# Kernel tuning notes

Hardware: AMD Instinct MI355X
Metric: run time of the kernel (lower is better)

The kernel has to match this reference:

```python
import jax, jax.numpy as jnp
import numpy as np

B, N, DIM, H, DH = 2, 4096, 512, 8, 64  # inner_dim = H*DH = 512


def setup_inputs() -> dict:
    key = jax.random.key(0)
    ks = jax.random.split(key, 4)
    x = jax.random.normal(ks[0], (B, N, DIM), dtype=jnp.float32)
    Wq = jax.random.normal(ks[1], (DIM, H * DH), dtype=jnp.float32) * (DIM ** -0.5)
    Wkv = jax.random.normal(ks[2], (DIM, 2 * H * DH), dtype=jnp.float32) * (DIM ** -0.5)
    Wo = jax.random.normal(ks[3], (H * DH, DIM), dtype=jnp.float32) * ((H * DH) ** -0.5)
    bo = jnp.zeros((DIM,), dtype=jnp.float32)
    return {"x": x, "Wq": Wq, "Wkv": Wkv, "Wo": Wo, "bo": bo}


def reference(x, Wq, Wkv, Wo, bo):
    scale = DH ** -0.5
    # projections (context defaults to x -> self-attention)
    q = x @ Wq
    kv = x @ Wkv
    k, v = jnp.split(kv, 2, axis=-1)
    # NOTE: original code scales q by dim_head**-0.5 in forward() AND again
    # inside attention(), i.e. an effective dim_head**-1 scaling. Faithful.
    q = q * scale
    # b n (h d) -> b h n d
    split_heads = lambda t: t.reshape(B, N, H, DH).transpose(0, 2, 1, 3)
    q, k, v = map(split_heads, (q, k, v))
    q = q * scale  # second scaling inside attention()
    sim = jnp.einsum('bhid,bhjd->bhij', q, k)  # [B,H,N,N] full score matrix
    sim = sim - jax.lax.stop_gradient(jnp.max(sim, axis=-1, keepdims=True))
    mask_value = -jnp.finfo(sim.dtype).max
    causal_mask = jnp.triu(jnp.ones((N, N), dtype=bool), k=1)
    sim = jnp.where(causal_mask, mask_value, sim)
    attn = jax.nn.softmax(sim, axis=-1)
    out = jnp.einsum('bhij,bhjd->bhid', attn, v)
    out = out.transpose(0, 2, 1, 3).reshape(B, N, H * DH)  # b h n d -> b n (h d)
    return out @ Wo + bo
```

## Files before the change

### kernel.cpp

```cpp
#include <hip/hip_runtime.h>

typedef short s16x8 __attribute__((ext_vector_type(8)));
typedef float f32x4 __attribute__((ext_vector_type(4)));
typedef unsigned short u16;
typedef unsigned int u32;

#define MFMA16(a, b, c) __builtin_amdgcn_mfma_f32_16x16x32_bf16((a), (b), (c), 0, 0, 0)

__device__ __forceinline__ u16 f2bf(float f) {
  u32 u = __float_as_uint(f);
  u += 0x7fffu + ((u >> 16) & 1u);
  return (u16)(u >> 16);
}
__device__ __forceinline__ u16 f2bf_fast(float f) {
  return (u16)((__float_as_uint(f) + 0x8000u) >> 16);
}
__device__ __forceinline__ float ex2(float x) {
  float r;
  asm("v_exp_f32 %0, %1" : "=v"(r) : "v"(x));
  return r;
}
__device__ __forceinline__ void gll(const u16* g, u16* l) {
  __builtin_amdgcn_global_load_lds((const __attribute__((address_space(1))) u32*)g,
                                   (__attribute__((address_space(3))) u32*)l, 16, 0, 0);
}

__global__ __launch_bounds__(256) void k_prep(const float* __restrict__ x,
                                              const float* __restrict__ Wq,
                                              const float* __restrict__ Wkv,
                                              const float* __restrict__ Wo,
                                              u16* __restrict__ xb,
                                              u16* __restrict__ wqkvt,
                                              u16* __restrict__ wot) {
  const int bx = blockIdx.x, t = threadIdx.x;
  if (bx < 4096) {
    int i = bx * 256 + t;
    float4 v = ((const float4*)x)[i];
    ushort4 o;
    o.x = f2bf(v.x); o.y = f2bf(v.y); o.z = f2bf(v.z); o.w = f2bf(v.w);
    ((ushort4*)xb)[i] = o;
    return;
  }
  __shared__ u16 tl[64 * 66];
  const float* src; u16* dst; int N, kb, nb;
  if (bx < 4160)      { int tb = bx - 4096; src = Wq;  dst = wqkvt;          N = 512;  kb = tb >> 3; nb = tb & 7; }
  else if (bx < 4288) { int tb = bx - 4160; src = Wkv; dst = wqkvt + 262144; N = 1024; kb = tb >> 4; nb = tb & 15; }
  else                { int tb = bx - 4288; src = Wo;  dst = wot;            N = 512;  kb = tb >> 3; nb = tb & 7; }
#pragma unroll
  for (int it = 0; it < 4; ++it) {
    int idx = it * 256 + t;
    int kl = idx >> 4, nc = idx & 15;
    float4 v = *(const float4*)(src + (kb * 64 + kl) * N + nb * 64 + nc * 4);
    u16* p = &tl[kl * 66 + nc * 4];
    p[0] = f2bf(v.x); p[1] = f2bf(v.y); p[2] = f2bf(v.z); p[3] = f2bf(v.w);
  }
  __syncthreads();
#pragma unroll
  for (int it = 0; it < 2; ++it) {
    int idx = it * 256 + t;
    int nl = idx >> 3, kc = idx & 7;
    u16 tmp[8];
#pragma unroll
    for (int j = 0; j < 8; ++j) tmp[j] = tl[(kc * 8 + j) * 66 + nl];
    *(s16x8*)(dst + (nb * 64 + nl) * 512 + kb * 64 + kc * 8) = *(const s16x8*)tmp;
  }
}

__global__ __launch_bounds__(256, 2) void k_gemm_qkv(
    const u16* __restrict__ A, const u16* __restrict__ Bt,
    u16* __restrict__ Qb, u16* __restrict__ Kb, u16* __restrict__ Vt) {
  __shared__ __align__(16) u16 As[8192], Bs[8192];
  const int t = threadIdx.x, w = t >> 6, l = t & 63, quad = l >> 4, lr = l & 15;
  const int bm = blockIdx.x, bn = blockIdx.y;
  const int wm = (w >> 1) * 64, wn = (w & 1) * 64;
  const f32x4 fz = {0.f, 0.f, 0.f, 0.f};
  f32x4 acc[4][4];
#pragma unroll
  for (int i = 0; i < 4; ++i)
#pragma unroll
    for (int j = 0; j < 4; ++j) acc[i][j] = fz;
  const u16* Ag = A + bm * 128 * 512;
  const u16* Bg = Bt + bn * 128 * 512;
  for (int kk = 0; kk < 8; ++kk) {
    __syncthreads();
#pragma unroll
    for (int i = 0; i < 4; ++i) {
      int ci = w * 256 + i * 64 + l;
      int row = ci >> 3, cb = ci & 7;
      int off = row * 512 + kk * 64 + ((cb ^ (row & 7)) << 3);
      gll(Ag + off, &As[w * 2048 + i * 512]);
      gll(Bg + off, &Bs[w * 2048 + i * 512]);
    }
    __syncthreads();
    s16x8 af[4][2], bf[4][2];
#pragma unroll
    for (int x2 = 0; x2 < 4; ++x2)
#pragma unroll
      for (int c = 0; c < 2; ++c) {
        int sw = ((c * 4 + quad) ^ (lr & 7)) << 3;
        af[x2][c] = *(const s16x8*)&As[(wm + x2 * 16 + lr) * 64 + sw];
        bf[x2][c] = *(const s16x8*)&Bs[(wn + x2 * 16 + lr) * 64 + sw];
      }
#pragma unroll
    for (int c = 0; c < 2; ++c)
#pragma unroll
      for (int ti = 0; ti < 4; ++ti)
#pragma unroll
        for (int tj = 0; tj < 4; ++tj)
          acc[ti][tj] = MFMA16(af[ti][c], bf[tj][c], acc[ti][tj]);
  }
  const int buf = (bn * 128) >> 9;
  const float QS = 0.0225421107f;
#pragma unroll
  for (int ti = 0; ti < 4; ++ti)
#pragma unroll
    for (int tj = 0; tj < 4; ++tj) {
      int col = bn * 128 + wn + tj * 16 + lr;
      int hd = col & 511, h = hd >> 6, d = hd & 63;
      int row0 = bm * 128 + wm + ti * 16 + quad * 4;
      int b = row0 >> 12, n0 = row0 & 4095;
      long base = (long)(b * 8 + h) * 262144;
      if (buf == 0) {
#pragma unroll
        for (int r = 0; r < 4; ++r) Qb[base + (long)(n0 + r) * 64 + d] = f2bf(acc[ti][tj][r] * QS);
      } else if (buf == 1) {
#pragma unroll
        for (int r = 0; r < 4; ++r) Kb[base + (long)(n0 + r) * 64 + d] = f2bf(acc[ti][tj][r]);
      } else {
        ushort4 pk;
        pk.x = f2bf(acc[ti][tj][0]); pk.y = f2bf(acc[ti][tj][1]);
        pk.z = f2bf(acc[ti][tj][2]); pk.w = f2bf(acc[ti][tj][3]);
        *(ushort4*)&Vt[base + (long)d * 4096 + n0] = pk;
      }
    }
}

__global__ __launch_bounds__(256, 2) void k_gemm_out(
    const u16* __restrict__ A, const u16* __restrict__ Bt,
    const float* __restrict__ bias, float* __restrict__ out) {
  __shared__ __align__(16) u16 As[8192], Bs[8192];
  const int t = threadIdx.x, w = t >> 6, l = t & 63, quad = l >> 4, lr = l & 15;
  const int bm = blockIdx.x, bn = blockIdx.y;
  const int wm = (w >> 1) * 64, wn = (w & 1) * 64;
  const f32x4 fz = {0.f, 0.f, 0.f, 0.f};
  f32x4 acc[4][4];
#pragma unroll
  for (int i = 0; i < 4; ++i)
#pragma unroll
    for (int j = 0; j < 4; ++j) acc[i][j] = fz;
  const u16* Ag = A + bm * 128 * 512;
  const u16* Bg = Bt + bn * 128 * 512;
  for (int kk = 0; kk < 8; ++kk) {
    __syncthreads();
#pragma unroll
    for (int i = 0; i < 4; ++i) {
      int ci = w * 256 + i * 64 + l;
      int row = ci >> 3, cb = ci & 7;
      int off = row * 512 + kk * 64 + ((cb ^ (row & 7)) << 3);
      gll(Ag + off, &As[w * 2048 + i * 512]);
      gll(Bg + off, &Bs[w * 2048 + i * 512]);
    }
    __syncthreads();
    s16x8 af[4][2], bf[4][2];
#pragma unroll
    for (int x2 = 0; x2 < 4; ++x2)
#pragma unroll
      for (int c = 0; c < 2; ++c) {
        int sw = ((c * 4 + quad) ^ (lr & 7)) << 3;
        af[x2][c] = *(const s16x8*)&As[(wm + x2 * 16 + lr) * 64 + sw];
        bf[x2][c] = *(const s16x8*)&Bs[(wn + x2 * 16 + lr) * 64 + sw];
      }
#pragma unroll
    for (int c = 0; c < 2; ++c)
#pragma unroll
      for (int ti = 0; ti < 4; ++ti)
#pragma unroll
        for (int tj = 0; tj < 4; ++tj)
          acc[ti][tj] = MFMA16(af[ti][c], bf[tj][c], acc[ti][tj]);
  }
#pragma unroll
  for (int ti = 0; ti < 4; ++ti)
#pragma unroll
    for (int tj = 0; tj < 4; ++tj) {
      int col = bn * 128 + wn + tj * 16 + lr;
      float bb = bias[col];
#pragma unroll
      for (int r = 0; r < 4; ++r) {
        int row = bm * 128 + wm + ti * 16 + quad * 4 + r;
        out[(long)row * 512 + col] = acc[ti][tj][r] + bb;
      }
    }
}

__global__ __launch_bounds__(128, 2) void k_attn(
    const u16* __restrict__ Qb, const u16* __restrict__ Kb,
    const u16* __restrict__ Vt, u16* __restrict__ Ob) {
  __shared__ __align__(16) u16 lds[12800];
  const int t = threadIdx.x, w = t >> 6, l = t & 63, quad = l >> 4, lr = l & 15;
  const int bid = blockIdx.x;
  const int qb = 63 - (bid >> 4), bh = bid & 15;
  const u16* Qh = Qb + (long)bh * 262144;
  const u16* Kh = Kb + (long)bh * 262144;
  const u16* Vh = Vt + (long)bh * 262144;
  const int q0 = qb * 64, rw0 = q0 + w * 32;
  s16x8 qf[2][2];
#pragma unroll
  for (int mt = 0; mt < 2; ++mt)
#pragma unroll
    for (int c = 0; c < 2; ++c)
      qf[mt][c] = *(const s16x8*)(Qh + (rw0 + mt * 16 + lr) * 64 + c * 32 + quad * 8);
  const f32x4 fz = {0.f, 0.f, 0.f, 0.f};
  f32x4 o[2][4];
#pragma unroll
  for (int mt = 0; mt < 2; ++mt)
#pragma unroll
    for (int nt = 0; nt < 4; ++nt) o[mt][nt] = fz;
  float m_r[2][4], l_r[2][4];
#pragma unroll
  for (int mt = 0; mt < 2; ++mt)
#pragma unroll
    for (int r = 0; r < 4; ++r) { m_r[mt][r] = -3.0e38f; l_r[mt][r] = 0.f; }
  u16* P = &lds[8192 + w * 2304];

  for (int jt = 0; jt <= qb; ++jt) {
    __syncthreads();
    const u16* Ksrc = Kh + jt * 4096;
    const u16* Vsrc = Vh + jt * 64;
#pragma unroll
    for (int i = 0; i < 4; ++i) {
      int ci = (w * 4 + i) * 64 + l;
      int row = ci >> 3, cb = ci & 7;
      int sw = (cb ^ (row & 7)) << 3;
      gll(Ksrc + row * 64 + sw, &lds[(w * 4 + i) * 512]);
      gll(Vsrc + row * 4096 + sw, &lds[4096 + (w * 4 + i) * 512]);
    }
    __syncthreads();
    f32x4 s[2][4];
#pragma unroll
    for (int mt = 0; mt < 2; ++mt)
#pragma unroll
      for (int nt = 0; nt < 4; ++nt) s[mt][nt] = fz;
#pragma unroll
    for (int c = 0; c < 2; ++c) {
      s16x8 kbf[4];
#pragma unroll
      for (int nt = 0; nt < 4; ++nt)
        kbf[nt] = *(const s16x8*)&lds[(nt * 16 + lr) * 64 + (((c * 4 + quad) ^ (lr & 7)) << 3)];
#pragma unroll
      for (int mt = 0; mt < 2; ++mt)
#pragma unroll
        for (int nt = 0; nt < 4; ++nt)
          s[mt][nt] = MFMA16(qf[mt][c], kbf[nt], s[mt][nt]);
    }
    const bool dg = (jt == qb);
#pragma unroll
    for (int mt = 0; mt < 2; ++mt) {
      if (dg) {
        int rloc = rw0 - jt * 64 + mt * 16 + quad * 4;
#pragma unroll
        for (int nt = 0; nt < 4; ++nt)
#pragma unroll
          for (int r = 0; r < 4; ++r)
            if (nt * 16 + lr > rloc + r) s[mt][nt][r] = -1e30f;
      }
      float al[4];
#pragma unroll
      for (int r = 0; r < 4; ++r) {
        float lm = fmaxf(fmaxf(s[mt][0][r], s[mt][1][r]), fmaxf(s[mt][2][r], s[mt][3][r]));
        lm = fmaxf(lm, __shfl_xor(lm, 1));
        lm = fmaxf(lm, __shfl_xor(lm, 2));
        lm = fmaxf(lm, __shfl_xor(lm, 4));
        lm = fmaxf(lm, __shfl_xor(lm, 8));
        float mn = fmaxf(m_r[mt][r], lm);
        al[r] = ex2(m_r[mt][r] - mn);
        m_r[mt][r] = mn;
      }
#pragma unroll
      for (int nt = 0; nt < 4; ++nt)
#pragma unroll
        for (int r = 0; r < 4; ++r) s[mt][nt][r] = ex2(s[mt][nt][r] - m_r[mt][r]);
#pragma unroll
      for (int r = 0; r < 4; ++r) {
        float ts = (s[mt][0][r] + s[mt][1][r]) + (s[mt][2][r] + s[mt][3][r]);
        ts += __shfl_xor(ts, 1);
        ts += __shfl_xor(ts, 2);
        ts += __shfl_xor(ts, 4);
        ts += __shfl_xor(ts, 8);
        l_r[mt][r] = l_r[mt][r] * al[r] + ts;
      }
#pragma unroll
      for (int nt = 0; nt < 4; ++nt)
#pragma unroll
        for (int r = 0; r < 4; ++r)
          P[(mt * 16 + quad * 4 + r) * 72 + nt * 16 + lr] = f2bf_fast(s[mt][nt][r]);
#pragma unroll
      for (int nt = 0; nt < 4; ++nt)
#pragma unroll
        for (int r = 0; r < 4; ++r) o[mt][nt][r] *= al[r];
    }
#pragma unroll
    for (int c = 0; c < 2; ++c) {
      s16x8 ap[2], bv[4];
#pragma unroll
      for (int mt = 0; mt < 2; ++mt)
        ap[mt] = *(const s16x8*)&P[(mt * 16 + lr) * 72 + c * 32 + quad * 8];
#pragma unroll
      for (int nt = 0; nt < 4; ++nt)
        bv[nt] = *(const s16x8*)&lds[4096 + (nt * 16 + lr) * 64 + (((c * 4 + quad) ^ (lr & 7)) << 3)];
#pragma unroll
      for (int mt = 0; mt < 2; ++mt)
#pragma unroll
        for (int nt = 0; nt < 4; ++nt)
          o[mt][nt] = MFMA16(ap[mt], bv[nt], o[mt][nt]);
    }
  }
#pragma unroll
  for (int mt = 0; mt < 2; ++mt) {
    float inv[4];
#pragma unroll
    for (int r = 0; r < 4; ++r) inv[r] = 1.0f / l_r[mt][r];
#pragma unroll
    for (int nt = 0; nt < 4; ++nt)
#pragma unroll
      for (int r = 0; r < 4; ++r)
        P[(mt * 16 + quad * 4 + r) * 72 + nt * 16 + lr] = f2bf(o[mt][nt][r] * inv[r]);
  }
  const int b = bh >> 3, h = bh & 7;
  const int row2 = l >> 1, half = l & 1;
  long gbase = (long)(b * 4096 + rw0 + row2) * 512 + h * 64 + half * 32;
  const u16* ps = &P[row2 * 72 + half * 32];
#pragma unroll
  for (int k = 0; k < 4; ++k)
    *(s16x8*)(Ob + gbase + k * 8) = *(const s16x8*)(ps + k * 8);
}

extern "C" void kernel_launch(void* const* d_in, const int* in_sizes, int n_in,
                              void* d_out, int out_size, void* d_ws, size_t ws_size,
                              hipStream_t stream) {
  const float* x   = (const float*)d_in[0];
  const float* Wq  = (const float*)d_in[1];
  const float* Wkv = (const float*)d_in[2];
  const float* Wo  = (const float*)d_in[3];
  const float* bo  = (const float*)d_in[4];
  float* out = (float*)d_out;
  char* ws = (char*)d_ws;
  u16* xbf   = (u16*)(ws + (0ull << 20));
  u16* wqkvt = (u16*)(ws + (8ull << 20));
  u16* wot   = (u16*)(ws + (10ull << 20));
  u16* Qb    = (u16*)(ws + (11ull << 20));
  u16* Kb    = (u16*)(ws + (19ull << 20));
  u16* Vtb   = (u16*)(ws + (27ull << 20));
  u16* Ob    = (u16*)(ws + (35ull << 20));

  k_prep<<<4352, 256, 0, stream>>>(x, Wq, Wkv, Wo, xbf, wqkvt, wot);
  k_gemm_qkv<<<dim3(64, 12), 256, 0, stream>>>(xbf, wqkvt, Qb, Kb, Vtb);
  k_attn<<<1024, 128, 0, stream>>>(Qb, Kb, Vtb, Ob);
  k_gemm_out<<<dim3(64, 4), 256, 0, stream>>>(Ob, wot, bo, out);
}
```

Baseline: 249.5 us.

## Double-buffer K/V tiles and widen attention blocks to 128 query rows

The attention kernel now uses 4 waves per block covering 128 query rows, so each K/V tile loaded into LDS is shared by twice as many queries, and the grid is halved. K/V tiles are double-buffered: the load of the next tile is issued before computing on the current one, removing one barrier per iteration and overlapping global loads with MFMA work. Waves whose rows lie entirely before a key tile skip the compute, and the causal mask condition is generalized per wave. LDS use doubles, which may limit occupancy, and work becomes less balanced across waves near the diagonal.

```diff
diff --git a/kernel.cpp b/kernel.cpp
--- a/kernel.cpp
+++ b/kernel.cpp
@@ -192,17 +192,18 @@
     }
 }
 
-__global__ __launch_bounds__(128, 2) void k_attn(
+__global__ __launch_bounds__(256, 2) void k_attn(
     const u16* __restrict__ Qb, const u16* __restrict__ Kb,
     const u16* __restrict__ Vt, u16* __restrict__ Ob) {
-  __shared__ __align__(16) u16 lds[12800];
+  __shared__ __align__(16) u16 lds[25600];
   const int t = threadIdx.x, w = t >> 6, l = t & 63, quad = l >> 4, lr = l & 15;
   const int bid = blockIdx.x;
-  const int qb = 63 - (bid >> 4), bh = bid & 15;
+  const int qt = 31 - (bid >> 4), bh = bid & 15;
   const u16* Qh = Qb + (long)bh * 262144;
   const u16* Kh = Kb + (long)bh * 262144;
   const u16* Vh = Vt + (long)bh * 262144;
-  const int q0 = qb * 64, rw0 = q0 + w * 32;
+  const int rw0 = qt * 128 + w * 32;
+  const int jend = 2 * qt + 1;
   s16x8 qf[2][2];
 #pragma unroll
   for (int mt = 0; mt < 2; ++mt)
@@ -220,21 +221,36 @@
   for (int mt = 0; mt < 2; ++mt)
 #pragma unroll
     for (int r = 0; r < 4; ++r) { m_r[mt][r] = -3.0e38f; l_r[mt][r] = 0.f; }
-  u16* P = &lds[8192 + w * 2304];
-
-  for (int jt = 0; jt <= qb; ++jt) {
-    __syncthreads();
-    const u16* Ksrc = Kh + jt * 4096;
-    const u16* Vsrc = Vh + jt * 64;
-#pragma unroll
-    for (int i = 0; i < 4; ++i) {
-      int ci = (w * 4 + i) * 64 + l;
-      int row = ci >> 3, cb = ci & 7;
+  u16* P = &lds[16384 + w * 2304];
+  const int ci0 = w * 128 + l;
+
+  {
+#pragma unroll
+    for (int i = 0; i < 2; ++i) {
+      int ci = ci0 + i * 64, row = ci >> 3, cb = ci & 7;
       int sw = (cb ^ (row & 7)) << 3;
-      gll(Ksrc + row * 64 + sw, &lds[(w * 4 + i) * 512]);
-      gll(Vsrc + row * 4096 + sw, &lds[4096 + (w * 4 + i) * 512]);
-    }
-    __syncthreads();
+      gll(Kh + row * 64 + sw, &lds[(w * 2 + i) * 512]);
+      gll(Vh + row * 4096 + sw, &lds[8192 + (w * 2 + i) * 512]);
+    }
+  }
+  for (int jt = 0; jt <= jend; ++jt) {
+    const int buf = jt & 1;
+    __syncthreads();
+    if (jt < jend) {
+      const u16* Ksrc = Kh + (jt + 1) * 4096;
+      const u16* Vsrc = Vh + (jt + 1) * 64;
+      const int nb = buf ^ 1;
+#pragma unroll
+      for (int i = 0; i < 2; ++i) {
+        int ci = ci0 + i * 64, row = ci >> 3, cb = ci & 7;
+        int sw = (cb ^ (row & 7)) << 3;
+        gll(Ksrc + row * 64 + sw, &lds[nb * 4096 + (w * 2 + i) * 512]);
+        gll(Vsrc + row * 4096 + sw, &lds[8192 + nb * 4096 + (w * 2 + i) * 512]);
+      }
+    }
+    if (jt * 64 >= rw0 + 32) continue;
+    const u16* Ks = &lds[buf * 4096];
+    const u16* Vs = &lds[8192 + buf * 4096];
     f32x4 s[2][4];
 #pragma unroll
     for (int mt = 0; mt < 2; ++mt)
@@ -245,14 +261,14 @@
       s16x8 kbf[4];
 #pragma unroll
       for (int nt = 0; nt < 4; ++nt)
-        kbf[nt] = *(const s16x8*)&lds[(nt * 16 + lr) * 64 + (((c * 4 + quad) ^ (lr & 7)) << 3)];
+        kbf[nt] = *(const s16x8*)&Ks[(nt * 16 + lr) * 64 + (((c * 4 + quad) ^ (lr & 7)) << 3)];
 #pragma unroll
       for (int mt = 0; mt < 2; ++mt)
 #pragma unroll
         for (int nt = 0; nt < 4; ++nt)
           s[mt][nt] = MFMA16(qf[mt][c], kbf[nt], s[mt][nt]);
     }
-    const bool dg = (jt == qb);
+    const bool dg = (jt * 64 + 63 > rw0);
 #pragma unroll
     for (int mt = 0; mt < 2; ++mt) {
       if (dg) {
@@ -306,7 +322,7 @@
         ap[mt] = *(const s16x8*)&P[(mt * 16 + lr) * 72 + c * 32 + quad * 8];
 #pragma unroll
       for (int nt = 0; nt < 4; ++nt)
-        bv[nt] = *(const s16x8*)&lds[4096 + (nt * 16 + lr) * 64 + (((c * 4 + quad) ^ (lr & 7)) << 3)];
+        bv[nt] = *(const s16x8*)&Vs[(nt * 16 + lr) * 64 + (((c * 4 + quad) ^ (lr & 7)) << 3)];
 #pragma unroll
       for (int mt = 0; mt < 2; ++mt)
 #pragma unroll
@@ -354,6 +370,6 @@
 
   k_prep<<<4352, 256, 0, stream>>>(x, Wq, Wkv, Wo, xbf, wqkvt, wot);
   k_gemm_qkv<<<dim3(64, 12), 256, 0, stream>>>(xbf, wqkvt, Qb, Kb, Vtb);
-  k_attn<<<1024, 128, 0, stream>>>(Qb, Kb, Vtb, Ob);
+  k_attn<<<512, 256, 0, stream>>>(Qb, Kb, Vtb, Ob);
   k_gemm_out<<<dim3(64, 4), 256, 0, stream>>>(Ob, wot, bo, out);
 }
```

Measured after the change: 266.3 us. +6.7%, slower.

## Split causal attention along KV into chunks with a separate combine kernel

Applied to the files above, without the earlier changes.

The attention kernel now splits each query tile's KV range into up to four 16-tile chunks (split-K / flash-decoding style). Partial outputs plus row max and sum go to workspace, and a new k_comb kernel merges them. This targets the load imbalance of causal attention, where late query tiles process 64 KV tiles while early ones process few. The kernel also computes S transposed so that P stays in registers and feeds a 16x16x16 MFMA, which removes the P round trip through LDS. V is stored in a pre-tiled layout, and waves skip fully masked tiles. The cost is an extra kernel launch, partial-result traffic through global memory, and bf16 rounding of the partial outputs.

```diff
diff --git a/kernel.cpp b/kernel.cpp
--- a/kernel.cpp
+++ b/kernel.cpp
@@ -1,11 +1,13 @@
 #include <hip/hip_runtime.h>
 
 typedef short s16x8 __attribute__((ext_vector_type(8)));
+typedef short s16x4 __attribute__((ext_vector_type(4)));
 typedef float f32x4 __attribute__((ext_vector_type(4)));
 typedef unsigned short u16;
 typedef unsigned int u32;
 
 #define MFMA16(a, b, c) __builtin_amdgcn_mfma_f32_16x16x32_bf16((a), (b), (c), 0, 0, 0)
+#define MFMA1616(a, b, c) __builtin_amdgcn_mfma_f32_16x16x16bf16_1k((a), (b), (c), 0, 0, 0)
 
 __device__ __forceinline__ u16 f2bf(float f) {
   u32 u = __float_as_uint(f);
@@ -14,6 +16,9 @@
 }
 __device__ __forceinline__ u16 f2bf_fast(float f) {
   return (u16)((__float_as_uint(f) + 0x8000u) >> 16);
+}
+__device__ __forceinline__ float bf2f(u16 u) {
+  return __uint_as_float(((u32)u) << 16);
 }
 __device__ __forceinline__ float ex2(float x) {
   float r;
@@ -68,7 +73,7 @@
 
 __global__ __launch_bounds__(256, 2) void k_gemm_qkv(
     const u16* __restrict__ A, const u16* __restrict__ Bt,
-    u16* __restrict__ Qb, u16* __restrict__ Kb, u16* __restrict__ Vt) {
+    u16* __restrict__ Qb, u16* __restrict__ Kb, u16* __restrict__ Vg) {
   __shared__ __align__(16) u16 As[8192], Bs[8192];
   const int t = threadIdx.x, w = t >> 6, l = t & 63, quad = l >> 4, lr = l & 15;
   const int bm = blockIdx.x, bn = blockIdx.y;
@@ -130,7 +135,9 @@
         ushort4 pk;
         pk.x = f2bf(acc[ti][tj][0]); pk.y = f2bf(acc[ti][tj][1]);
         pk.z = f2bf(acc[ti][tj][2]); pk.w = f2bf(acc[ti][tj][3]);
-        *(ushort4*)&Vt[base + (long)d * 4096 + n0] = pk;
+        long vaddr = base + ((long)((n0 >> 6) * 4 + ((n0 >> 4) & 3)) * 4 + (d >> 4)) * 256
+                     + (long)(d & 15) * 16 + (n0 & 15);
+        *(ushort4*)&Vg[vaddr] = pk;
       }
     }
 }
@@ -192,146 +199,183 @@
     }
 }
 
-__global__ __launch_bounds__(128, 2) void k_attn(
+__global__ __launch_bounds__(128, 3) void k_attn_split(
     const u16* __restrict__ Qb, const u16* __restrict__ Kb,
-    const u16* __restrict__ Vt, u16* __restrict__ Ob) {
-  __shared__ __align__(16) u16 lds[12800];
+    const u16* __restrict__ Vg, u16* __restrict__ pO,
+    float* __restrict__ pM, float* __restrict__ pL) {
+  const int bid = blockIdx.x;
+  const int qt = 63 - (bid >> 6), rem = bid & 63, bh = rem >> 2, c = rem & 3;
+  const int jcount = qt + 1;
+  const int nc = (jcount + 15) >> 4;
+  if (c >= nc) return;
+  const int jstart = c * 16;
+  const int jendx = (jstart + 16 < jcount) ? jstart + 16 : jcount;
+  __shared__ __align__(16) u16 lds[8192];
   const int t = threadIdx.x, w = t >> 6, l = t & 63, quad = l >> 4, lr = l & 15;
-  const int bid = blockIdx.x;
-  const int qb = 63 - (bid >> 4), bh = bid & 15;
   const u16* Qh = Qb + (long)bh * 262144;
   const u16* Kh = Kb + (long)bh * 262144;
-  const u16* Vh = Vt + (long)bh * 262144;
-  const int q0 = qb * 64, rw0 = q0 + w * 32;
+  const u16* Vh = Vg + (long)bh * 262144;
+  const int rw0 = qt * 64 + w * 32;
   s16x8 qf[2][2];
 #pragma unroll
   for (int mt = 0; mt < 2; ++mt)
 #pragma unroll
-    for (int c = 0; c < 2; ++c)
-      qf[mt][c] = *(const s16x8*)(Qh + (rw0 + mt * 16 + lr) * 64 + c * 32 + quad * 8);
+    for (int cc = 0; cc < 2; ++cc)
+      qf[mt][cc] = *(const s16x8*)(Qh + (rw0 + mt * 16 + lr) * 64 + cc * 32 + quad * 8);
   const f32x4 fz = {0.f, 0.f, 0.f, 0.f};
   f32x4 o[2][4];
 #pragma unroll
   for (int mt = 0; mt < 2; ++mt)
 #pragma unroll
-    for (int nt = 0; nt < 4; ++nt) o[mt][nt] = fz;
-  float m_r[2][4], l_r[2][4];
-#pragma unroll
-  for (int mt = 0; mt < 2; ++mt)
-#pragma unroll
-    for (int r = 0; r < 4; ++r) { m_r[mt][r] = -3.0e38f; l_r[mt][r] = 0.f; }
-  u16* P = &lds[8192 + w * 2304];
-
-  for (int jt = 0; jt <= qb; ++jt) {
+    for (int dt = 0; dt < 4; ++dt) o[mt][dt] = fz;
+  float m_r[2] = {-3.0e38f, -3.0e38f};
+  float lp[2] = {0.f, 0.f};
+
+  for (int jt = jstart; jt < jendx; ++jt) {
     __syncthreads();
     const u16* Ksrc = Kh + jt * 4096;
-    const u16* Vsrc = Vh + jt * 64;
+    const u16* Vsrc = Vh + jt * 4096;
 #pragma unroll
     for (int i = 0; i < 4; ++i) {
       int ci = (w * 4 + i) * 64 + l;
       int row = ci >> 3, cb = ci & 7;
       int sw = (cb ^ (row & 7)) << 3;
       gll(Ksrc + row * 64 + sw, &lds[(w * 4 + i) * 512]);
-      gll(Vsrc + row * 4096 + sw, &lds[4096 + (w * 4 + i) * 512]);
-    }
-    __syncthreads();
+      gll(Vsrc + ci * 8, &lds[4096 + (w * 4 + i) * 512]);
+    }
+    __syncthreads();
+    if (jt * 64 >= rw0 + 32) continue;
     f32x4 s[2][4];
 #pragma unroll
     for (int mt = 0; mt < 2; ++mt)
 #pragma unroll
       for (int nt = 0; nt < 4; ++nt) s[mt][nt] = fz;
 #pragma unroll
-    for (int c = 0; c < 2; ++c) {
+    for (int cc = 0; cc < 2; ++cc) {
       s16x8 kbf[4];
 #pragma unroll
       for (int nt = 0; nt < 4; ++nt)
-        kbf[nt] = *(const s16x8*)&lds[(nt * 16 + lr) * 64 + (((c * 4 + quad) ^ (lr & 7)) << 3)];
+        kbf[nt] = *(const s16x8*)&lds[(nt * 16 + lr) * 64 + (((cc * 4 + quad) ^ (lr & 7)) << 3)];
 #pragma unroll
       for (int mt = 0; mt < 2; ++mt)
 #pragma unroll
         for (int nt = 0; nt < 4; ++nt)
-          s[mt][nt] = MFMA16(qf[mt][c], kbf[nt], s[mt][nt]);
-    }
-    const bool dg = (jt == qb);
+          s[mt][nt] = MFMA16(kbf[nt], qf[mt][cc], s[mt][nt]);
+    }
+    const bool dg = (jt * 64 + 63 > rw0);
+    s16x4 pf[2][4];
 #pragma unroll
     for (int mt = 0; mt < 2; ++mt) {
       if (dg) {
-        int rloc = rw0 - jt * 64 + mt * 16 + quad * 4;
+        int T = rw0 + mt * 16 + lr - jt * 64;
 #pragma unroll
         for (int nt = 0; nt < 4; ++nt)
 #pragma unroll
           for (int r = 0; r < 4; ++r)
-            if (nt * 16 + lr > rloc + r) s[mt][nt][r] = -1e30f;
-      }
-      float al[4];
-#pragma unroll
-      for (int r = 0; r < 4; ++r) {
-        float lm = fmaxf(fmaxf(s[mt][0][r], s[mt][1][r]), fmaxf(s[mt][2][r], s[mt][3][r]));
-        lm = fmaxf(lm, __shfl_xor(lm, 1));
-        lm = fmaxf(lm, __shfl_xor(lm, 2));
-        lm = fmaxf(lm, __shfl_xor(lm, 4));
-        lm = fmaxf(lm, __shfl_xor(lm, 8));
-        float mn = fmaxf(m_r[mt][r], lm);
-        al[r] = ex2(m_r[mt][r] - mn);
-        m_r[mt][r] = mn;
-      }
+            if (nt * 16 + quad * 4 + r > T) s[mt][nt][r] = -1e30f;
+      }
+      float lm = fmaxf(fmaxf(fmaxf(s[mt][0][0], s[mt][0][1]), fmaxf(s[mt][0][2], s[mt][0][3])),
+                       fmaxf(fmaxf(s[mt][1][0], s[mt][1][1]), fmaxf(s[mt][1][2], s[mt][1][3])));
+      float lm2 = fmaxf(fmaxf(fmaxf(s[mt][2][0], s[mt][2][1]), fmaxf(s[mt][2][2], s[mt][2][3])),
+                        fmaxf(fmaxf(s[mt][3][0], s[mt][3][1]), fmaxf(s[mt][3][2], s[mt][3][3])));
+      lm = fmaxf(lm, lm2);
+      lm = fmaxf(lm, __shfl_xor(lm, 16));
+      lm = fmaxf(lm, __shfl_xor(lm, 32));
+      float mn = fmaxf(m_r[mt], lm);
+      float al = ex2(m_r[mt] - mn);
+      m_r[mt] = mn;
+      float ts = 0.f;
 #pragma unroll
       for (int nt = 0; nt < 4; ++nt)
 #pragma unroll
-        for (int r = 0; r < 4; ++r) s[mt][nt][r] = ex2(s[mt][nt][r] - m_r[mt][r]);
-#pragma unroll
-      for (int r = 0; r < 4; ++r) {
-        float ts = (s[mt][0][r] + s[mt][1][r]) + (s[mt][2][r] + s[mt][3][r]);
-        ts += __shfl_xor(ts, 1);
-        ts += __shfl_xor(ts, 2);
-        ts += __shfl_xor(ts, 4);
-        ts += __shfl_xor(ts, 8);
-        l_r[mt][r] = l_r[mt][r] * al[r] + ts;
-      }
-#pragma unroll
-      for (int nt = 0; nt < 4; ++nt)
-#pragma unroll
-        for (int r = 0; r < 4; ++r)
-          P[(mt * 16 + quad * 4 + r) * 72 + nt * 16 + lr] = f2bf_fast(s[mt][nt][r]);
-#pragma unroll
-      for (int nt = 0; nt < 4; ++nt)
-#pragma unroll
-        for (int r = 0; r < 4; ++r) o[mt][nt][r] *= al[r];
-    }
-#pragma unroll
-    for (int c = 0; c < 2; ++c) {
-      s16x8 ap[2], bv[4];
+        for (int r = 0; r < 4; ++r) {
+          float p = ex2(s[mt][nt][r] - mn);
+          s[mt][nt][r] = p;
+          ts += p;
+        }
+      lp[mt] = lp[mt] * al + ts;
+#pragma unroll
+      for (int nt = 0; nt < 4; ++nt) {
+        s16x4 pk;
+        pk[0] = (short)f2bf_fast(s[mt][nt][0]);
+        pk[1] = (short)f2bf_fast(s[mt][nt][1]);
+        pk[2] = (short)f2bf_fast(s[mt][nt][2]);
+        pk[3] = (short)f2bf_fast(s[mt][nt][3]);
+        pf[mt][nt] = pk;
+      }
+#pragma unroll
+      for (int dt = 0; dt < 4; ++dt)
+#pragma unroll
+        for (int r = 0; r < 4; ++r) o[mt][dt][r] *= al;
+    }
+#pragma unroll
+    for (int nt = 0; nt < 4; ++nt) {
+      s16x4 av[4];
+#pragma unroll
+      for (int dt = 0; dt < 4; ++dt)
+        av[dt] = *(const s16x4*)&lds[4096 + (nt * 4 + dt) * 256 + lr * 16 + quad * 4];
 #pragma unroll
       for (int mt = 0; mt < 2; ++mt)
-        ap[mt] = *(const s16x8*)&P[(mt * 16 + lr) * 72 + c * 32 + quad * 8];
-#pragma unroll
-      for (int nt = 0; nt < 4; ++nt)
-        bv[nt] = *(const s16x8*)&lds[4096 + (nt * 16 + lr) * 64 + (((c * 4 + quad) ^ (lr & 7)) << 3)];
-#pragma unroll
-      for (int mt = 0; mt < 2; ++mt)
-#pragma unroll
-        for (int nt = 0; nt < 4; ++nt)
-          o[mt][nt] = MFMA16(ap[mt], bv[nt], o[mt][nt]);
-    }
-  }
+#pragma unroll
+        for (int dt = 0; dt < 4; ++dt)
+          o[mt][dt] = MFMA1616(av[dt], pf[mt][nt], o[mt][dt]);
+    }
+  }
+  const int pidx = (bh * 64 + qt) * 4 + c;
 #pragma unroll
   for (int mt = 0; mt < 2; ++mt) {
-    float inv[4];
-#pragma unroll
-    for (int r = 0; r < 4; ++r) inv[r] = 1.0f / l_r[mt][r];
-#pragma unroll
-    for (int nt = 0; nt < 4; ++nt)
-#pragma unroll
-      for (int r = 0; r < 4; ++r)
-        P[(mt * 16 + quad * 4 + r) * 72 + nt * 16 + lr] = f2bf(o[mt][nt][r] * inv[r]);
-  }
+    float lv = lp[mt];
+    lv += __shfl_xor(lv, 16);
+    lv += __shfl_xor(lv, 32);
+    if (quad == 0) {
+      pM[pidx * 64 + w * 32 + mt * 16 + lr] = m_r[mt];
+      pL[pidx * 64 + w * 32 + mt * 16 + lr] = lv;
+    }
+#pragma unroll
+    for (int dt = 0; dt < 4; ++dt) {
+      ushort4 pk;
+      pk.x = f2bf(o[mt][dt][0]); pk.y = f2bf(o[mt][dt][1]);
+      pk.z = f2bf(o[mt][dt][2]); pk.w = f2bf(o[mt][dt][3]);
+      *(ushort4*)&pO[(long)pidx * 4096 + (w * 32 + mt * 16 + lr) * 64 + dt * 16 + quad * 4] = pk;
+    }
+  }
+}
+
+__global__ __launch_bounds__(128) void k_comb(const u16* __restrict__ pO,
+                                              const float* __restrict__ pM,
+                                              const float* __restrict__ pL,
+                                              u16* __restrict__ Ob) {
+  const int bid = blockIdx.x, t = threadIdx.x;
+  const int bh = bid >> 6, qt = bid & 63;
+  const int nc = (qt + 16) >> 4;
+  const int row = t >> 1, half = t & 1;
+  const int pbase = (bh * 64 + qt) * 4;
+  float M = -3.0e38f;
+  for (int c = 0; c < nc; ++c) M = fmaxf(M, pM[(pbase + c) * 64 + row]);
+  float L = 0.f;
+  float acc[32];
+#pragma unroll
+  for (int d = 0; d < 32; ++d) acc[d] = 0.f;
+  for (int c = 0; c < nc; ++c) {
+    float wgt = ex2(pM[(pbase + c) * 64 + row] - M);
+    L += pL[(pbase + c) * 64 + row] * wgt;
+    const u16* src = pO + (long)(pbase + c) * 4096 + row * 64 + half * 32;
+#pragma unroll
+    for (int k = 0; k < 4; ++k) {
+      s16x8 v = *(const s16x8*)(src + k * 8);
+#pragma unroll
+      for (int j = 0; j < 8; ++j) acc[k * 8 + j] += wgt * bf2f((u16)v[j]);
+    }
+  }
+  float inv = 1.0f / L;
+  u16 tmp[32];
+#pragma unroll
+  for (int d = 0; d < 32; ++d) tmp[d] = f2bf(acc[d] * inv);
   const int b = bh >> 3, h = bh & 7;
-  const int row2 = l >> 1, half = l & 1;
-  long gbase = (long)(b * 4096 + rw0 + row2) * 512 + h * 64 + half * 32;
-  const u16* ps = &P[row2 * 72 + half * 32];
+  long gbase = (long)(b * 4096 + qt * 64 + row) * 512 + h * 64 + half * 32;
 #pragma unroll
   for (int k = 0; k < 4; ++k)
-    *(s16x8*)(Ob + gbase + k * 8) = *(const s16x8*)(ps + k * 8);
+    *(s16x8*)(Ob + gbase + k * 8) = *(const s16x8*)(tmp + k * 8);
 }
 
 extern "C" void kernel_launch(void* const* d_in, const int* in_sizes, int n_in,
@@ -344,16 +388,21 @@
   const float* bo  = (const float*)d_in[4];
   float* out = (float*)d_out;
   char* ws = (char*)d_ws;
-  u16* xbf   = (u16*)(ws + (0ull << 20));
-  u16* wqkvt = (u16*)(ws + (8ull << 20));
-  u16* wot   = (u16*)(ws + (10ull << 20));
-  u16* Qb    = (u16*)(ws + (11ull << 20));
-  u16* Kb    = (u16*)(ws + (19ull << 20));
-  u16* Vtb   = (u16*)(ws + (27ull << 20));
-  u16* Ob    = (u16*)(ws + (35ull << 20));
+  const size_t MB = 1048576;
+  u16* wot   = (u16*)(ws);
+  u16* wqkvt = (u16*)(ws + MB / 2);
+  u16* Qb    = (u16*)(ws + 2 * MB);
+  u16* Kb    = (u16*)(ws + 10 * MB);
+  u16* Vg    = (u16*)(ws + 18 * MB);
+  u16* Ob    = (u16*)(ws + 26 * MB);
+  u16* xbf   = (u16*)(ws + 34 * MB);
+  u16* pO    = (u16*)(ws + 34 * MB);
+  float* pM  = (float*)(ws + 66 * MB);
+  float* pL  = (float*)(ws + 67 * MB);
 
   k_prep<<<4352, 256, 0, stream>>>(x, Wq, Wkv, Wo, xbf, wqkvt, wot);
-  k_gemm_qkv<<<dim3(64, 12), 256, 0, stream>>>(xbf, wqkvt, Qb, Kb, Vtb);
-  k_attn<<<1024, 128, 0, stream>>>(Qb, Kb, Vtb, Ob);
+  k_gemm_qkv<<<dim3(64, 12), 256, 0, stream>>>(xbf, wqkvt, Qb, Kb, Vg);
+  k_attn_split<<<4096, 128, 0, stream>>>(Qb, Kb, Vg, pO, pM, pL);
+  k_comb<<<1024, 128, 0, stream>>>(pO, pM, pL, Ob);
   k_gemm_out<<<dim3(64, 4), 256, 0, stream>>>(Ob, wot, bo, out);
 }
```

After: 219.6 us. 12.0% less time.
